# Optimization experiments

Hardware: AMD Instinct MI355X
Metric: run time of the kernel (lower is better)

Reference implementation:

```python
import jax, jax.numpy as jnp
import numpy as np

SIZE = 512
ATTN = 64      # per-head attention_size
OUT = 64       # per-head output_size
HEADS = 8

def setup_inputs() -> dict:
    key = jax.random.key(0)
    ks = jax.random.split(key, 7)
    s = 0.02
    return {
        "x":  jax.random.normal(ks[0], (4, 2048, SIZE), dtype=jnp.float32),
        "Wq": jax.random.normal(ks[1], (SIZE, ATTN * HEADS), dtype=jnp.float32) * s,
        "bq": jax.random.normal(ks[2], (ATTN * HEADS,), dtype=jnp.float32) * s,
        "Wk": jax.random.normal(ks[3], (SIZE, ATTN), dtype=jnp.float32) * s,  # shared key, no bias
        "Wv": jax.random.normal(ks[4], (SIZE, OUT * HEADS), dtype=jnp.float32) * s,
        "bv": jax.random.normal(ks[5], (OUT * HEADS,), dtype=jnp.float32) * s,
    }

def reference(x, Wq, bq, Wk, Wv, bv):
    B, S, _ = x.shape
    q = (x @ Wq + bq).reshape(B, S, HEADS, ATTN)   # (B,S,H,A)
    k = x @ Wk                                      # (B,S,A) shared across heads
    v = (x @ Wv + bv).reshape(B, S, HEADS, OUT)     # (B,S,H,O)
    # NOTE: original divides by sqrt(seq_len), not sqrt(head_dim)
    scale = 1.0 / np.sqrt(S).astype(np.float32)
    scores = jnp.einsum("bqha,bka->bhqk", q, k) * scale  # (B,H,S,S)
    causal = jnp.tril(jnp.ones((S, S), dtype=bool))
    scores = jnp.where(causal, scores, -jnp.inf)
    attn = jax.nn.softmax(scores, axis=-1)
    out = jnp.einsum("bhqk,bkho->bqho", attn, v)    # (B,S,H,O)
    return out.reshape(B, S, HEADS * OUT)
```

## Files before the change

kernel.cpp:

```cpp
#include <hip/hip_runtime.h>
#include <math.h>


typedef _Float16 half8 __attribute__((ext_vector_type(8)));
typedef _Float16 half4 __attribute__((ext_vector_type(4)));
typedef float float4v __attribute__((ext_vector_type(4)));
typedef unsigned int u32;

#define SCL2E 0.031885926f

__device__ inline float4v mfma16(half8 a, half8 b, float4v c) {
    return __builtin_amdgcn_mfma_f32_16x16x32_f16(a, b, c, 0, 0, 0);
}
__device__ inline void load16(const _Float16* g, _Float16* l) {
    __builtin_amdgcn_global_load_lds((const __attribute__((address_space(1))) u32*)g,
                                     (__attribute__((address_space(3))) u32*)l, 16, 0, 0);
}

__global__ __launch_bounds__(256) void prep(
    const float* __restrict__ x, const float* __restrict__ Wq,
    const float* __restrict__ Wk, const float* __restrict__ Wv,
    _Float16* __restrict__ xh, _Float16* __restrict__ wqt,
    _Float16* __restrict__ wkt, _Float16* __restrict__ wvt) {
    const int bid = blockIdx.x;
    if (bid < 2048) {
        size_t base = (size_t)bid * 2048 + (size_t)threadIdx.x * 8;
        const float4* xp = (const float4*)(x + base);
        float4 f0 = xp[0], f1 = xp[1];
        half8 h = {(_Float16)f0.x, (_Float16)f0.y, (_Float16)f0.z, (_Float16)f0.w,
                   (_Float16)f1.x, (_Float16)f1.y, (_Float16)f1.z, (_Float16)f1.w};
        *(half8*)(xh + base) = h;
    } else {
        int r = bid - 2048;
        const float* W; _Float16* WT; int N, bx, by;
        if (r < 256)      { W = Wq; WT = wqt; N = 512; bx = r & 15; by = r >> 4; }
        else if (r < 288) { r -= 256; W = Wk; WT = wkt; N = 64;  bx = r & 1;  by = r >> 1; }
        else              { r -= 288; W = Wv; WT = wvt; N = 512; bx = r & 15; by = r >> 4; }
        __shared__ float T[32][33];
        const int tx = threadIdx.x & 31, ty = threadIdx.x >> 5;
        const int n0 = bx * 32, k0 = by * 32;
#pragma unroll
        for (int i = 0; i < 4; ++i)
            T[ty + 8 * i][tx] = W[(size_t)(k0 + ty + 8 * i) * N + n0 + tx];
        __syncthreads();
#pragma unroll
        for (int i = 0; i < 4; ++i)
            WT[(size_t)(n0 + ty + 8 * i) * 512 + k0 + tx] = (_Float16)T[tx][ty + 8 * i];
    }
}

__global__ __launch_bounds__(256) void qkv_gemm(
    const _Float16* __restrict__ xh,
    const _Float16* __restrict__ wqt, const _Float16* __restrict__ wkt,
    const _Float16* __restrict__ wvt,
    const float* __restrict__ bq, const float* __restrict__ bv,
    _Float16* __restrict__ q_ws, _Float16* __restrict__ kt_ws, _Float16* __restrict__ vt_ws) {
    __shared__ __align__(16) _Float16 Xs[8192];
    __shared__ __align__(16) _Float16 Ws[4096];

    const int m0 = blockIdx.x * 128;
    const int nt = blockIdx.y;
    const _Float16* WT;
    const float* bias;
    if (nt < 8)       { WT = wqt + (size_t)nt * 64 * 512; bias = bq + nt * 64; }
    else if (nt == 8) { WT = wkt;                          bias = nullptr; }
    else              { WT = wvt + (size_t)(nt - 9) * 64 * 512; bias = bv + (nt - 9) * 64; }

    const int tid = threadIdx.x;
    const int w = tid >> 6, lane = tid & 63, quad = lane >> 4, cl = lane & 15;
    const int lrow = lane >> 3;
    const int lgc = (lane & 7) ^ lrow;
    const _Float16* xg = xh + (size_t)(m0 + lrow) * 512 + lgc * 8;
    const _Float16* wg = WT + (size_t)lrow * 512 + lgc * 8;

    const int g0 = (quad ^ (cl & 7)) << 3;
    const int g1 = ((quad ^ 4) ^ (cl & 7)) << 3;

    float4v acc[2][4] = {};

    for (int ki = 0; ki < 8; ++ki) {
        const int kk = ki * 64;
        __syncthreads();
#pragma unroll
        for (int c = 0; c < 4; ++c) {
            int cc = w * 4 + c;
            load16(xg + (size_t)cc * 8 * 512 + kk, Xs + cc * 512);
        }
#pragma unroll
        for (int c = 0; c < 2; ++c) {
            int cc = w * 2 + c;
            load16(wg + (size_t)cc * 8 * 512 + kk, Ws + cc * 512);
        }
        __syncthreads();
#pragma unroll
        for (int c = 0; c < 2; ++c) {
            const int g = c ? g1 : g0;
#pragma unroll
            for (int s = 0; s < 2; ++s) {
                half8 a = *(const half8*)(Xs + (w * 32 + s * 16 + cl) * 64 + g);
#pragma unroll
                for (int j = 0; j < 4; ++j) {
                    half8 b = *(const half8*)(Ws + (j * 16 + cl) * 64 + g);
                    acc[s][j] = mfma16(a, b, acc[s][j]);
                }
            }
        }
    }

    if (nt < 8) {
#pragma unroll
        for (int s = 0; s < 2; ++s)
#pragma unroll
            for (int j = 0; j < 4; ++j)
#pragma unroll
                for (int r = 0; r < 4; ++r) {
                    int lr = w * 32 + s * 16 + quad * 4 + r;
                    int col = j * 16 + cl;
                    q_ws[(size_t)(m0 + lr) * 512 + nt * 64 + col] =
                        (_Float16)((acc[s][j][r] + bias[col]) * SCL2E);
                }
    } else if (nt == 8) {
#pragma unroll
        for (int s = 0; s < 2; ++s)
#pragma unroll
            for (int j = 0; j < 4; ++j)
#pragma unroll
                for (int r = 0; r < 4; ++r) {
                    int grow = m0 + w * 32 + s * 16 + quad * 4 + r;
                    int b = grow >> 11, t = (grow >> 6) & 31, row = grow & 63;
                    int col = j * 16 + cl;
                    kt_ws[((size_t)(b * 32 + t) << 12) + row * 64 +
                          (((col >> 3) ^ (row & 7)) << 3) + (col & 7)] = (_Float16)acc[s][j][r];
                }
    } else {
        const int h = nt - 9;
#pragma unroll
        for (int s = 0; s < 2; ++s)
#pragma unroll
            for (int j = 0; j < 4; ++j)
#pragma unroll
                for (int r = 0; r < 4; ++r) {
                    int grow = m0 + w * 32 + s * 16 + quad * 4 + r;
                    int b = grow >> 11, t = (grow >> 6) & 31, row = grow & 63;
                    int o = j * 16 + cl;
                    int kap = ((row & 15) << 2) + (row >> 4);
                    vt_ws[(((size_t)(b * 8 + h) * 32 + t) << 12) + o * 64 +
                          (((kap >> 3) ^ (o & 7)) << 3) + (kap & 7)] =
                        (_Float16)(acc[s][j][r] + bias[o]);
                }
    }
}

__global__ __launch_bounds__(512) void attn(
    const _Float16* __restrict__ q_ws, const _Float16* __restrict__ kt_ws,
    const _Float16* __restrict__ vt_ws, float* __restrict__ out) {
    __shared__ __align__(16) _Float16 Ks[4096];
    __shared__ __align__(16) _Float16 VTs[2][4096];
    __shared__ __align__(16) _Float16 Ps[8][1024];

    const int bh = blockIdx.x, b = bh >> 3, h = bh & 7;
    const int pair = blockIdx.y;
    const int bS = b * 2048;
    const int tid = threadIdx.x;
    const int w = tid >> 6, lane = tid & 63, quad = lane >> 4, cl = lane & 15;

    const _Float16* kbase = kt_ws + ((size_t)(b * 32) << 12);
    const _Float16* vbase = vt_ws + ((size_t)((b * 8 + h) * 32) << 12);

    const int g0 = (quad ^ (cl & 7)) << 3;
    const int g1 = ((quad ^ 4) ^ (cl & 7)) << 3;
    const int soff = w * 512 + lane * 8;

    for (int phase = 0; phase < 2; ++phase) {
        const int qt = phase ? (15 - pair) : pair;
        const int tlast = 2 * qt + 1;
        const int q0 = qt * 128;

        const _Float16* qbase = q_ws + (size_t)(bS + q0 + w * 16 + cl) * 512 + h * 64;
        half8 qa0 = *(const half8*)(qbase + quad * 8);
        half8 qa1 = *(const half8*)(qbase + 32 + quad * 8);

        float4v oacc[4] = {};
        float l_run[4] = {0.f, 0.f, 0.f, 0.f};

        load16(kbase + soff, &Ks[w * 512]);
        load16(vbase + soff, &VTs[0][w * 512]);

        for (int t = 0; t <= tlast; ++t) {
            __syncthreads();
            if (t < tlast) {
                load16(vbase + ((size_t)(t + 1) << 12) + soff, &VTs[(t + 1) & 1][w * 512]);
            }
            const int ww = (t == tlast) ? (w - 4) : ((t == 2 * qt) ? w : 100);
            if (ww >= 0) {
                const int jmax = ww < 3 ? ww : 3;
                float4v sfr[4];
#pragma unroll
                for (int j = 0; j < 4; ++j) {
                    if (j <= jmax) {
                        const _Float16* kr = &Ks[(j * 16 + cl) * 64];
                        half8 b0 = *(const half8*)(kr + g0);
                        half8 b1 = *(const half8*)(kr + g1);
                        float4v a_ = {0.f, 0.f, 0.f, 0.f};
                        a_ = mfma16(qa0, b0, a_);
                        a_ = mfma16(qa1, b1, a_);
                        sfr[j] = a_;
                    }
                }
#pragma unroll
                for (int r = 0; r < 4; ++r) {
                    float pj[4];
#pragma unroll
                    for (int j = 0; j < 4; ++j) {
                        bool live = (j < jmax) ||
                                    (j == jmax && (ww > 3 || cl <= quad * 4 + r));
                        pj[j] = live ? exp2f(sfr[j][r]) : 0.f;
                    }
                    l_run[r] += (pj[0] + pj[1]) + (pj[2] + pj[3]);
                    int rr = quad * 4 + r;
                    half4 ph = {(_Float16)pj[0], (_Float16)pj[1], (_Float16)pj[2], (_Float16)pj[3]};
                    *(half4*)&Ps[w][rr * 64 + ((((cl >> 1) ^ (rr & 7)) << 3) | ((cl & 1) << 2))] = ph;
                }
            }
            __syncthreads();
            if (t < tlast) {
                load16(kbase + ((size_t)(t + 1) << 12) + soff, &Ks[w * 512]);
            }
            if (ww >= 0) {
                const _Float16* PB = &Ps[w][cl * 64];
                half8 pa0 = *(const half8*)(PB + g0);
                half8 pa1 = *(const half8*)(PB + g1);
                const int bb = t & 1;
#pragma unroll
                for (int jo = 0; jo < 4; ++jo) {
                    const _Float16* vr = &VTs[bb][(jo * 16 + cl) * 64];
                    half8 v0 = *(const half8*)(vr + g0);
                    half8 v1 = *(const half8*)(vr + g1);
                    oacc[jo] = mfma16(pa0, v0, oacc[jo]);
                    oacc[jo] = mfma16(pa1, v1, oacc[jo]);
                }
            }
        }
#pragma unroll
        for (int r = 0; r < 4; ++r) {
            float l = l_run[r];
            l += __shfl_xor(l, 1);
            l += __shfl_xor(l, 2);
            l += __shfl_xor(l, 4);
            l += __shfl_xor(l, 8);
            float inv = 1.0f / l;
            int row = q0 + w * 16 + quad * 4 + r;
            float* op = out + (size_t)(bS + row) * 512 + h * 64 + cl;
            op[0]  = oacc[0][r] * inv;
            op[16] = oacc[1][r] * inv;
            op[32] = oacc[2][r] * inv;
            op[48] = oacc[3][r] * inv;
        }
    }
}

extern "C" void kernel_launch(void* const* d_in, const int* in_sizes, int n_in,
                              void* d_out, int out_size, void* d_ws, size_t ws_size,
                              hipStream_t stream) {
    const float* x  = (const float*)d_in[0];
    const float* Wq = (const float*)d_in[1];
    const float* bq = (const float*)d_in[2];
    const float* Wk = (const float*)d_in[3];
    const float* Wv = (const float*)d_in[4];
    const float* bv = (const float*)d_in[5];
    float* out = (float*)d_out;

    char* ws = (char*)d_ws;
    _Float16* q_ws  = (_Float16*)(ws);
    _Float16* kt_ws = (_Float16*)(ws + 8388608);
    _Float16* vt_ws = (_Float16*)(ws + 9437184);
    _Float16* wqt   = (_Float16*)(ws + 17825792);
    _Float16* wkt   = (_Float16*)(ws + 18350080);
    _Float16* wvt   = (_Float16*)(ws + 18415616);
    _Float16* xh    = (_Float16*)(ws + 18939904);

    prep<<<dim3(2592), dim3(256), 0, stream>>>(x, Wq, Wk, Wv, xh, wqt, wkt, wvt);

    qkv_gemm<<<dim3(64, 17), dim3(256), 0, stream>>>(
        xh, wqt, wkt, wvt, bq, bv, q_ws, kt_ws, vt_ws);

    attn<<<dim3(32, 8), dim3(512), 0, stream>>>(q_ws, kt_ws, vt_ws, out);
}
```

Before: 149.3 us.

## Split attention into 64-row query blocks with 256 threads, heavy-first order

The attention kernel drops the paired-phase scheme, where each 512-thread block handled two 128-row query tiles in sequence. Each block now handles one 64-row query slice with 4 waves, and the grid grows from 32x8 to 32x32 blocks. Blocks are ordered so the longest causal slices start first, and launch bounds ask for 4 blocks per CU. The goal is more parallelism and occupancy with less idle time from masking, at the cost of loading the K/V tiles more times from global memory and more syncs per unit of work.

```diff
diff --git a/kernel.cpp b/kernel.cpp
--- a/kernel.cpp
+++ b/kernel.cpp
@@ -151,15 +151,23 @@
     }
 }
 
-__global__ __launch_bounds__(512) void attn(
+__global__ __launch_bounds__(256, 4) void attn(
     const _Float16* __restrict__ q_ws, const _Float16* __restrict__ kt_ws,
     const _Float16* __restrict__ vt_ws, float* __restrict__ out) {
     __shared__ __align__(16) _Float16 Ks[4096];
     __shared__ __align__(16) _Float16 VTs[2][4096];
-    __shared__ __align__(16) _Float16 Ps[8][1024];
+    __shared__ __align__(16) _Float16 Ps[4][1024];
 
     const int bh = blockIdx.x, b = bh >> 3, h = bh & 7;
-    const int pair = blockIdx.y;
+    const int y = blockIdx.y;
+    int qt, half;
+    if (y < 8)       { qt = 15 - y; half = 1; }
+    else if (y < 16) { qt = y - 8;  half = 1; }
+    else if (y < 24) { qt = 31 - y; half = 0; }
+    else             { qt = y - 24; half = 0; }
+    const int tlast = 2 * qt + half;
+    const int q0 = qt * 128 + half * 64;
+
     const int bS = b * 2048;
     const int tid = threadIdx.x;
     const int w = tid >> 6, lane = tid & 63, quad = lane >> 4, cl = lane & 15;
@@ -169,93 +177,88 @@
 
     const int g0 = (quad ^ (cl & 7)) << 3;
     const int g1 = ((quad ^ 4) ^ (cl & 7)) << 3;
-    const int soff = w * 512 + lane * 8;
-
-    for (int phase = 0; phase < 2; ++phase) {
-        const int qt = phase ? (15 - pair) : pair;
-        const int tlast = 2 * qt + 1;
-        const int q0 = qt * 128;
-
-        const _Float16* qbase = q_ws + (size_t)(bS + q0 + w * 16 + cl) * 512 + h * 64;
-        half8 qa0 = *(const half8*)(qbase + quad * 8);
-        half8 qa1 = *(const half8*)(qbase + 32 + quad * 8);
-
-        float4v oacc[4] = {};
-        float l_run[4] = {0.f, 0.f, 0.f, 0.f};
-
-        load16(kbase + soff, &Ks[w * 512]);
-        load16(vbase + soff, &VTs[0][w * 512]);
-
-        for (int t = 0; t <= tlast; ++t) {
-            __syncthreads();
-            if (t < tlast) {
-                load16(vbase + ((size_t)(t + 1) << 12) + soff, &VTs[(t + 1) & 1][w * 512]);
+    const int so0 = w * 1024 + lane * 8;
+
+    const _Float16* qbase = q_ws + (size_t)(bS + q0 + w * 16 + cl) * 512 + h * 64;
+    half8 qa0 = *(const half8*)(qbase + quad * 8);
+    half8 qa1 = *(const half8*)(qbase + 32 + quad * 8);
+
+    float4v oacc[4] = {};
+    float l_run[4] = {0.f, 0.f, 0.f, 0.f};
+
+    load16(kbase + so0,       &Ks[w * 1024]);
+    load16(kbase + so0 + 512, &Ks[w * 1024 + 512]);
+    load16(vbase + so0,       &VTs[0][w * 1024]);
+    load16(vbase + so0 + 512, &VTs[0][w * 1024 + 512]);
+
+    for (int t = 0; t <= tlast; ++t) {
+        __syncthreads();
+        if (t < tlast) {
+            const _Float16* vt = vbase + ((size_t)(t + 1) << 12);
+            load16(vt + so0,       &VTs[(t + 1) & 1][w * 1024]);
+            load16(vt + so0 + 512, &VTs[(t + 1) & 1][w * 1024 + 512]);
+        }
+        const int ww = (t == tlast) ? w : 100;
+        const int jmax = ww < 3 ? ww : 3;
+        float4v sfr[4];
+#pragma unroll
+        for (int j = 0; j < 4; ++j) {
+            if (j <= jmax) {
+                const _Float16* kr = &Ks[(j * 16 + cl) * 64];
+                half8 b0 = *(const half8*)(kr + g0);
+                half8 b1 = *(const half8*)(kr + g1);
+                float4v a_ = {0.f, 0.f, 0.f, 0.f};
+                a_ = mfma16(qa0, b0, a_);
+                a_ = mfma16(qa1, b1, a_);
+                sfr[j] = a_;
             }
-            const int ww = (t == tlast) ? (w - 4) : ((t == 2 * qt) ? w : 100);
-            if (ww >= 0) {
-                const int jmax = ww < 3 ? ww : 3;
-                float4v sfr[4];
-#pragma unroll
-                for (int j = 0; j < 4; ++j) {
-                    if (j <= jmax) {
-                        const _Float16* kr = &Ks[(j * 16 + cl) * 64];
-                        half8 b0 = *(const half8*)(kr + g0);
-                        half8 b1 = *(const half8*)(kr + g1);
-                        float4v a_ = {0.f, 0.f, 0.f, 0.f};
-                        a_ = mfma16(qa0, b0, a_);
-                        a_ = mfma16(qa1, b1, a_);
-                        sfr[j] = a_;
-                    }
-                }
-#pragma unroll
-                for (int r = 0; r < 4; ++r) {
-                    float pj[4];
-#pragma unroll
-                    for (int j = 0; j < 4; ++j) {
-                        bool live = (j < jmax) ||
-                                    (j == jmax && (ww > 3 || cl <= quad * 4 + r));
-                        pj[j] = live ? exp2f(sfr[j][r]) : 0.f;
-                    }
-                    l_run[r] += (pj[0] + pj[1]) + (pj[2] + pj[3]);
-                    int rr = quad * 4 + r;
-                    half4 ph = {(_Float16)pj[0], (_Float16)pj[1], (_Float16)pj[2], (_Float16)pj[3]};
-                    *(half4*)&Ps[w][rr * 64 + ((((cl >> 1) ^ (rr & 7)) << 3) | ((cl & 1) << 2))] = ph;
-                }
+        }
+#pragma unroll
+        for (int r = 0; r < 4; ++r) {
+            float pj[4];
+#pragma unroll
+            for (int j = 0; j < 4; ++j) {
+                bool live = (j < jmax) || (j == jmax && (ww > 3 || cl <= quad * 4 + r));
+                pj[j] = live ? exp2f(sfr[j][r]) : 0.f;
             }
-            __syncthreads();
-            if (t < tlast) {
-                load16(kbase + ((size_t)(t + 1) << 12) + soff, &Ks[w * 512]);
-            }
-            if (ww >= 0) {
-                const _Float16* PB = &Ps[w][cl * 64];
-                half8 pa0 = *(const half8*)(PB + g0);
-                half8 pa1 = *(const half8*)(PB + g1);
-                const int bb = t & 1;
-#pragma unroll
-                for (int jo = 0; jo < 4; ++jo) {
-                    const _Float16* vr = &VTs[bb][(jo * 16 + cl) * 64];
-                    half8 v0 = *(const half8*)(vr + g0);
-                    half8 v1 = *(const half8*)(vr + g1);
-                    oacc[jo] = mfma16(pa0, v0, oacc[jo]);
-                    oacc[jo] = mfma16(pa1, v1, oacc[jo]);
-                }
-            }
-        }
-#pragma unroll
-        for (int r = 0; r < 4; ++r) {
-            float l = l_run[r];
-            l += __shfl_xor(l, 1);
-            l += __shfl_xor(l, 2);
-            l += __shfl_xor(l, 4);
-            l += __shfl_xor(l, 8);
-            float inv = 1.0f / l;
-            int row = q0 + w * 16 + quad * 4 + r;
-            float* op = out + (size_t)(bS + row) * 512 + h * 64 + cl;
-            op[0]  = oacc[0][r] * inv;
-            op[16] = oacc[1][r] * inv;
-            op[32] = oacc[2][r] * inv;
-            op[48] = oacc[3][r] * inv;
-        }
+            l_run[r] += (pj[0] + pj[1]) + (pj[2] + pj[3]);
+            int rr = quad * 4 + r;
+            half4 ph = {(_Float16)pj[0], (_Float16)pj[1], (_Float16)pj[2], (_Float16)pj[3]};
+            *(half4*)&Ps[w][rr * 64 + ((((cl >> 1) ^ (rr & 7)) << 3) | ((cl & 1) << 2))] = ph;
+        }
+        __syncthreads();
+        if (t < tlast) {
+            const _Float16* kt = kbase + ((size_t)(t + 1) << 12);
+            load16(kt + so0,       &Ks[w * 1024]);
+            load16(kt + so0 + 512, &Ks[w * 1024 + 512]);
+        }
+        const _Float16* PB = &Ps[w][cl * 64];
+        half8 pa0 = *(const half8*)(PB + g0);
+        half8 pa1 = *(const half8*)(PB + g1);
+        const int bb = t & 1;
+#pragma unroll
+        for (int jo = 0; jo < 4; ++jo) {
+            const _Float16* vr = &VTs[bb][(jo * 16 + cl) * 64];
+            half8 v0 = *(const half8*)(vr + g0);
+            half8 v1 = *(const half8*)(vr + g1);
+            oacc[jo] = mfma16(pa0, v0, oacc[jo]);
+            oacc[jo] = mfma16(pa1, v1, oacc[jo]);
+        }
+    }
+#pragma unroll
+    for (int r = 0; r < 4; ++r) {
+        float l = l_run[r];
+        l += __shfl_xor(l, 1);
+        l += __shfl_xor(l, 2);
+        l += __shfl_xor(l, 4);
+        l += __shfl_xor(l, 8);
+        float inv = 1.0f / l;
+        int row = q0 + w * 16 + quad * 4 + r;
+        float* op = out + (size_t)(bS + row) * 512 + h * 64 + cl;
+        op[0]  = oacc[0][r] * inv;
+        op[16] = oacc[1][r] * inv;
+        op[32] = oacc[2][r] * inv;
+        op[48] = oacc[3][r] * inv;
     }
 }
 
@@ -284,5 +287,5 @@
     qkv_gemm<<<dim3(64, 17), dim3(256), 0, stream>>>(
         xh, wqt, wkt, wvt, bq, bv, q_ws, kt_ws, vt_ws);
 
-    attn<<<dim3(32, 8), dim3(512), 0, stream>>>(q_ws, kt_ws, vt_ws, out);
-}
+    attn<<<dim3(32, 32), dim3(256), 0, stream>>>(q_ws, kt_ws, vt_ws, out);
+}
```

Measured after the change: 144.9 us. -2.9%, faster.
